# Kernel optimization log

Measured on AMD Instinct MI355X. Metric: run time of the kernel, lower is better.

The kernel has to match this reference:

```python
import jax, jax.numpy as jnp
import numpy as np

DIM = 256
NUM_HEADS = 4
HEAD_DIM = DIM // NUM_HEADS
WINDOW_SIZES = [2, 4, 8, 16]
SCALE = HEAD_DIM ** -0.5


def setup_inputs() -> dict:
    key = jax.random.key(0)
    k1, k2, k3, k4 = jax.random.split(key, 4)
    B, C, H, W = 8, DIM, 128, 128
    x = jax.random.normal(k1, (B, C, H, W), dtype=jnp.float32)
    # 1x1 conv weights stored as [out, in]
    qkv_w = jax.random.normal(k2, (3 * DIM, DIM), dtype=jnp.float32) * (DIM ** -0.5)
    proj_w = jax.random.normal(k3, (DIM, DIM), dtype=jnp.float32) * (DIM ** -0.5)
    proj_b = jax.random.normal(k4, (DIM,), dtype=jnp.float32) * 0.01
    return {"x": x, "qkv_w": qkv_w, "proj_w": proj_w, "proj_b": proj_b}


def _window_attn(q, k, v, ws):
    # q,k,v: [B, H, W, hd] for one head; windowed self-attention of size ws
    B, H, W, hd = q.shape
    hg, wg = H // ws, W // ws

    def part(t):
        # [B,H,W,hd] -> [B, hg*wg, ws*ws, hd]
        t = t.reshape(B, hg, ws, wg, ws, hd).transpose(0, 1, 3, 2, 4, 5)
        return t.reshape(B, hg * wg, ws * ws, hd)

    qw, kw, vw = part(q), part(k), part(v)
    attn = jnp.einsum('bgqd,bgkd->bgqk', qw, kw) * SCALE
    attn = jax.nn.softmax(attn, axis=-1)
    out = jnp.einsum('bgqk,bgkd->bgqd', attn, vw)
    # reassemble: [B, hg, wg, ws, ws, hd] -> [B, H, W, hd]
    out = out.reshape(B, hg, wg, ws, ws, hd).transpose(0, 1, 3, 2, 4, 5)
    return out.reshape(B, H, W, hd)


def reference(x, qkv_w, proj_w, proj_b):
    B, C, H, W = x.shape
    # 1x1 conv qkv: [B, 3*dim, H, W] -> [3, B, nh, H, W, hd]
    qkv = jnp.einsum('bchw,oc->bohw', x, qkv_w)
    qkv = qkv.reshape(B, 3, NUM_HEADS, HEAD_DIM, H, W).transpose(1, 0, 2, 4, 5, 3)
    q, k, v = qkv[0], qkv[1], qkv[2]
    outs = []
    for i, ws in enumerate(WINDOW_SIZES):
        outs.append(_window_attn(q[:, i], k[:, i], v[:, i], ws))
    y = jnp.concatenate(outs, axis=-1)  # [B, H, W, dim]
    y = jnp.einsum('bhwc,oc->bhwo', y, proj_w) + proj_b
    y = y.transpose(0, 3, 1, 2)  # [B, dim, H, W]
    return y + x
```

## Files before the change

### kernel.cpp

```cpp
#include <hip/hip_runtime.h>
#include <hip/hip_bf16.h>
#include <cstddef>
#include <cstdint>

typedef unsigned short u16;
typedef unsigned int uint32;
typedef __attribute__((ext_vector_type(8))) short bf16x8;
typedef __attribute__((ext_vector_type(4))) float f32x4;

#define SPATIAL 16384
#define TOTAL_M 131072

__device__ __forceinline__ u16 f2b(float f) {
  __hip_bfloat16 h = __float2bfloat16(f);
  return *reinterpret_cast<u16*>(&h);
}
__device__ __forceinline__ uint32 pk2(float a, float b) {
  return (uint32)f2b(a) | ((uint32)f2b(b) << 16);
}
__device__ __forceinline__ float blo(uint32 u) {
  union { uint32 u; float f; } c; c.u = u << 16; return c.f;
}
__device__ __forceinline__ float bhi(uint32 u) {
  union { uint32 u; float f; } c; c.u = u & 0xffff0000u; return c.f;
}

__device__ __forceinline__ void gload_lds16(const u16* g, u16* l) {
  __builtin_amdgcn_global_load_lds(
      (const __attribute__((address_space(1))) void*)g,
      (__attribute__((address_space(3))) void*)l, 16, 0, 0);
}

template <int WS>
__device__ __forceinline__ size_t tok_base(int gw, int tt) {
  constexpr int WG = 128 / WS;
  constexpr int NWIN = WG * WG;
  int bb = gw / NWIN, rr = gw % NWIN;
  int gy = rr / WG, gx = rr % WG;
  int yy = gy * WS + tt / WS, xx = gx * WS + tt % WS;
  return (((size_t)bb * 128 + yy) * 128 + xx) * 768;
}

__global__ __launch_bounds__(256) void wprep(const float* __restrict__ qw,
                                             const float* __restrict__ pw,
                                             u16* __restrict__ wq,
                                             u16* __restrict__ wp) {
  const int t = blockIdx.x * 256 + threadIdx.x;
#pragma unroll
  for (int i = 0; i < 16; ++i) {
    const int e = i * 4096 + t;
    if (e < 49152) {
      float4 v = *(const float4*)&qw[(size_t)e * 4];
      ushort4 o;
      o.x = f2b(v.x); o.y = f2b(v.y); o.z = f2b(v.z); o.w = f2b(v.w);
      *(ushort4*)&wq[(size_t)e * 4] = o;
    } else {
      float4 v = *(const float4*)&pw[(size_t)(e - 49152) * 4];
      ushort4 o;
      o.x = f2b(v.x); o.y = f2b(v.y); o.z = f2b(v.z); o.w = f2b(v.w);
      *(ushort4*)&wp[(size_t)(e - 49152) * 4] = o;
    }
  }
}

__global__ __launch_bounds__(256) void gemm_qkv(const float* __restrict__ x,
                                                const u16* __restrict__ wq,
                                                u16* __restrict__ qkv) {
  __shared__ u16 As[128 * 64];
  __shared__ u16 Bs[128 * 64];
  const int tid = threadIdx.x;
  const int bid = blockIdx.x;
  const int logical = (bid & 7) * 768 + (bid >> 3);
  const int m0 = (logical / 6) * 128;
  const int n0 = (logical % 6) * 128;
  const int b = m0 >> 14;
  const int sp0 = m0 & 16383;
  const int lane = tid & 63, w = tid >> 6;
  const int wr = w >> 1, wc = w & 1;
  const int fr = lane & 15, fk = lane >> 4;
  const int frx = (fr & 7) << 3;
  const int kcs = ((tid & 7) * 8) ^ (((tid >> 3) & 7) << 3);
  const int srow = tid >> 3;
  const int spq = tid & 31;
  const int kq8 = tid >> 5;
  f32x4 acc[4][4] = {};
  for (int kt = 0; kt < 4; ++kt) {
    const int k0 = kt * 64;
#pragma unroll
    for (int it = 0; it < 4; ++it) {
      int row = it * 32 + srow;
      u16* lb = &Bs[(it * 256 + (tid & 192)) * 8];
      gload_lds16(&wq[((size_t)(n0 + row) << 8) + k0 + kcs], lb);
    }
    float4 xa[8];
#pragma unroll
    for (int j = 0; j < 8; ++j)
      xa[j] = *(const float4*)&x[(((size_t)(b * 256 + k0 + kq8 * 8 + j)) << 14) + sp0 + spq * 4];
#pragma unroll
    for (int s = 0; s < 4; ++s) {
      const int sp = spq * 4 + s;
      union { bf16x8 v; uint32 u[4]; } U;
      U.u[0] = pk2(((const float*)&xa[0])[s], ((const float*)&xa[1])[s]);
      U.u[1] = pk2(((const float*)&xa[2])[s], ((const float*)&xa[3])[s]);
      U.u[2] = pk2(((const float*)&xa[4])[s], ((const float*)&xa[5])[s]);
      U.u[3] = pk2(((const float*)&xa[6])[s], ((const float*)&xa[7])[s]);
      const int ch = kq8 ^ (sp & 7);
      *(bf16x8*)&As[sp * 64 + ch * 8] = U.v;
    }
    __syncthreads();
#pragma unroll
    for (int kk = 0; kk < 2; ++kk) {
      const int kb = (kk * 32 + fk * 8) ^ frx;
      bf16x8 af[4], bfr[4];
#pragma unroll
      for (int i = 0; i < 4; ++i) {
        af[i] = *(const bf16x8*)&As[(wr * 64 + i * 16 + fr) * 64 + kb];
        bfr[i] = *(const bf16x8*)&Bs[(wc * 64 + i * 16 + fr) * 64 + kb];
      }
#pragma unroll
      for (int i = 0; i < 4; ++i)
#pragma unroll
        for (int j = 0; j < 4; ++j)
          acc[i][j] = __builtin_amdgcn_mfma_f32_16x16x32_bf16(bfr[j], af[i], acc[i][j], 0, 0, 0);
    }
    __syncthreads();
  }
#pragma unroll
  for (int i = 0; i < 4; ++i) {
    const size_t row = (size_t)(m0 + wr * 64 + i * 16 + fr) * 768;
#pragma unroll
    for (int j = 0; j < 4; ++j) {
      uint2 p;
      p.x = pk2(acc[i][j][0], acc[i][j][1]);
      p.y = pk2(acc[i][j][2], acc[i][j][3]);
      *(uint2*)&qkv[row + n0 + wc * 64 + j * 16 + fk * 4] = p;
    }
  }
}

template <int WS>
__device__ __forceinline__ void win_attn_body(u16* __restrict__ qkv, int head,
                                              int bid, u16 (*Ks)[68], u16 (*Vs)[68]) {
  constexpr int T = WS * WS;
  constexpr int G = 256 / T;
  const int tid = threadIdx.x;
  const int gw0 = bid * G;
  const int qoff = head * 64;

#pragma unroll
  for (int i = 0; i < 16; ++i) {
    int e4 = i * 256 + tid;
    int tok = e4 >> 4;
    int d4 = (e4 & 15) * 4;
    size_t base = tok_base<WS>(gw0 + tok / T, tok % T);
    *(uint2*)&Ks[tok][d4] = *(const uint2*)&qkv[base + 256 + qoff + d4];
    *(uint2*)&Vs[tok][d4] = *(const uint2*)&qkv[base + 512 + qoff + d4];
  }
  __syncthreads();

  const int myw = tid / T;
  const int mytt = tid % T;
  const size_t mybase = tok_base<WS>(gw0 + myw, mytt);

  float q[64];
#pragma unroll
  for (int d4 = 0; d4 < 16; ++d4) {
    uint2 q2 = *(const uint2*)&qkv[mybase + qoff + d4 * 4];
    q[d4 * 4 + 0] = blo(q2.x); q[d4 * 4 + 1] = bhi(q2.x);
    q[d4 * 4 + 2] = blo(q2.y); q[d4 * 4 + 3] = bhi(q2.y);
  }
  const int rbase = myw * T;

  float mmax = -1e30f, lsum = 0.f;
  for (int j = 0; j < T; ++j) {
    float s = 0.f;
#pragma unroll
    for (int d4 = 0; d4 < 16; ++d4) {
      uint2 k2 = *(const uint2*)&Ks[rbase + j][d4 * 4];
      s = fmaf(q[d4 * 4 + 0], blo(k2.x), s);
      s = fmaf(q[d4 * 4 + 1], bhi(k2.x), s);
      s = fmaf(q[d4 * 4 + 2], blo(k2.y), s);
      s = fmaf(q[d4 * 4 + 3], bhi(k2.y), s);
    }
    s *= 0.125f;
    const float mn = fmaxf(mmax, s);
    lsum = lsum * __expf(mmax - mn) + __expf(s - mn);
    mmax = mn;
  }
  const float inv = 1.f / lsum;

  float acc[64] = {};
  for (int j = 0; j < T; ++j) {
    float s = 0.f;
#pragma unroll
    for (int d4 = 0; d4 < 16; ++d4) {
      uint2 k2 = *(const uint2*)&Ks[rbase + j][d4 * 4];
      s = fmaf(q[d4 * 4 + 0], blo(k2.x), s);
      s = fmaf(q[d4 * 4 + 1], bhi(k2.x), s);
      s = fmaf(q[d4 * 4 + 2], blo(k2.y), s);
      s = fmaf(q[d4 * 4 + 3], bhi(k2.y), s);
    }
    const float p = __expf(s * 0.125f - mmax) * inv;
#pragma unroll
    for (int d4 = 0; d4 < 16; ++d4) {
      uint2 v2 = *(const uint2*)&Vs[rbase + j][d4 * 4];
      acc[d4 * 4 + 0] = fmaf(p, blo(v2.x), acc[d4 * 4 + 0]);
      acc[d4 * 4 + 1] = fmaf(p, bhi(v2.x), acc[d4 * 4 + 1]);
      acc[d4 * 4 + 2] = fmaf(p, blo(v2.y), acc[d4 * 4 + 2]);
      acc[d4 * 4 + 3] = fmaf(p, bhi(v2.y), acc[d4 * 4 + 3]);
    }
  }
#pragma unroll
  for (int d4 = 0; d4 < 16; ++d4) {
    uint2 o2;
    o2.x = pk2(acc[d4 * 4 + 0], acc[d4 * 4 + 1]);
    o2.y = pk2(acc[d4 * 4 + 2], acc[d4 * 4 + 3]);
    *(uint2*)&qkv[mybase + qoff + d4 * 4] = o2;
  }
}

__global__ __launch_bounds__(256) void win_small(u16* __restrict__ qkv) {
  __shared__ u16 Ks[256][68];
  __shared__ u16 Vs[256][68];
  if (blockIdx.x < 512)
    win_attn_body<2>(qkv, 0, blockIdx.x, Ks, Vs);
  else
    win_attn_body<4>(qkv, 1, blockIdx.x - 512, Ks, Vs);
}

template <int WS>
__global__ __launch_bounds__(256) void win_attn_mfma(u16* __restrict__ qkv, int head) {
  constexpr int T = WS * WS;
  constexpr int G = 256 / T;
  constexpr int KT = T / 16;
  constexpr int KS = T / 32;
  constexpr int PL = T + 8;
  __shared__ u16 Ks[256 * 72];
  __shared__ u16 Vt[64 * 264];
  __shared__ u16 Plds[4 * 16 * PL];
  const int tid = threadIdx.x;
  const int gw0 = blockIdx.x * G;
  const int qoff = head * 64;

#pragma unroll
  for (int it = 0; it < 16; ++it) {
    int e = it * 256 + tid;
    int tok = e >> 4;
    int d4 = (e & 15) * 4;
    int win = tok / T, tt = tok % T;
    size_t base = tok_base<WS>(gw0 + win, tt);
    uint2 kk = *(const uint2*)&qkv[base + 256 + qoff + d4];
    uint2 vv = *(const uint2*)&qkv[base + 512 + qoff + d4];
    *(uint2*)&Ks[tok * 72 + d4] = kk;
    Vt[(d4 + 0) * 264 + tok] = (u16)(vv.x & 0xffffu);
    Vt[(d4 + 1) * 264 + tok] = (u16)(vv.x >> 16);
    Vt[(d4 + 2) * 264 + tok] = (u16)(vv.y & 0xffffu);
    Vt[(d4 + 3) * 264 + tok] = (u16)(vv.y >> 16);
  }
  __syncthreads();

  const int w = tid >> 6, lane = tid & 63;
  const int fr = lane & 15, fk = lane >> 4;
  u16* prow = &Plds[(w * 16 + fr) * PL];

  for (int qi = 0; qi < 4; ++qi) {
    const int qg = w * 4 + qi;
    const int win = qg / (T / 16);
    const int qt = qg % (T / 16);
    const int gw = gw0 + win;

    const size_t qb = tok_base<WS>(gw, qt * 16 + fr) + qoff;
    bf16x8 qf[2];
#pragma unroll
    for (int ds = 0; ds < 2; ++ds)
      qf[ds] = *(const bf16x8*)&qkv[qb + ds * 32 + fk * 8];

    f32x4 sv[KT];
#pragma unroll
    for (int kt = 0; kt < KT; ++kt) {
      const u16* krow = &Ks[(win * T + kt * 16 + fr) * 72];
      bf16x8 k0 = *(const bf16x8*)&krow[fk * 8];
      bf16x8 k1 = *(const bf16x8*)&krow[32 + fk * 8];
      f32x4 s = {};
      s = __builtin_amdgcn_mfma_f32_16x16x32_bf16(k0, qf[0], s, 0, 0, 0);
      s = __builtin_amdgcn_mfma_f32_16x16x32_bf16(k1, qf[1], s, 0, 0, 0);
      sv[kt] = s;
    }

    float rmax = -3e38f;
#pragma unroll
    for (int kt = 0; kt < KT; ++kt)
#pragma unroll
      for (int r = 0; r < 4; ++r) rmax = fmaxf(rmax, sv[kt][r]);
    rmax = fmaxf(rmax, __shfl_xor(rmax, 16));
    rmax = fmaxf(rmax, __shfl_xor(rmax, 32));
    const float m = rmax * 0.125f;
    float l = 0.f;
#pragma unroll
    for (int kt = 0; kt < KT; ++kt)
#pragma unroll
      for (int r = 0; r < 4; ++r) {
        float ev = __expf(sv[kt][r] * 0.125f - m);
        sv[kt][r] = ev;
        l += ev;
      }
    l += __shfl_xor(l, 16);
    l += __shfl_xor(l, 32);
    const float linv = 1.f / l;

#pragma unroll
    for (int kt = 0; kt < KT; ++kt) {
      uint2 pp;
      pp.x = pk2(sv[kt][0], sv[kt][1]);
      pp.y = pk2(sv[kt][2], sv[kt][3]);
      *(uint2*)&prow[kt * 16 + fk * 4] = pp;
    }
    __asm__ __volatile__("s_waitcnt lgkmcnt(0)" ::: "memory");
    __builtin_amdgcn_sched_barrier(0);

    f32x4 ov[4] = {};
#pragma unroll
    for (int ks = 0; ks < KS; ++ks) {
      bf16x8 pf = *(const bf16x8*)&prow[ks * 32 + fk * 8];
#pragma unroll
      for (int dt = 0; dt < 4; ++dt) {
        bf16x8 vf = *(const bf16x8*)&Vt[(dt * 16 + fr) * 264 + win * T + ks * 32 + fk * 8];
        ov[dt] = __builtin_amdgcn_mfma_f32_16x16x32_bf16(pf, vf, ov[dt], 0, 0, 0);
      }
    }

#pragma unroll
    for (int r = 0; r < 4; ++r) {
      float lr = __shfl(linv, fk * 4 + r);
      size_t ob = tok_base<WS>(gw, qt * 16 + fk * 4 + r) + qoff;
#pragma unroll
      for (int dt = 0; dt < 4; ++dt)
        qkv[ob + dt * 16 + fr] = f2b(ov[dt][r] * lr);
    }
  }
}

__global__ __launch_bounds__(256) void gemm_proj(const u16* __restrict__ qkv,
                                                 const u16* __restrict__ wp,
                                                 const float* __restrict__ bias,
                                                 const float* __restrict__ x,
                                                 float* __restrict__ out) {
  __shared__ u16 As[2][128 * 64];
  __shared__ u16 Bs[2][128 * 64];
  const int tid = threadIdx.x;
  const int bid = blockIdx.x;
  const int logical = (bid & 7) * 256 + (bid >> 3);
  const int m0 = (logical >> 1) * 128;
  const int n0 = (logical & 1) * 128;
  const int lane = tid & 63, w = tid >> 6;
  const int wr = w >> 1, wc = w & 1;
  const int fr = lane & 15, fk = lane >> 4;
  const int frx = (fr & 7) << 3;
  const int kcs = ((tid & 7) * 8) ^ (((tid >> 3) & 7) << 3);
  const int srow = tid >> 3;
  const int b = m0 >> 14;
  f32x4 acc[4][4] = {};

#define STAGE_PRJ(B, KT)                                                     \
  do {                                                                       \
    const int k0s = (KT)*64;                                                 \
    _Pragma("unroll") for (int it = 0; it < 4; ++it) {                       \
      int row = it * 32 + srow;                                              \
      u16* la = &As[B][(it * 256 + (tid & 192)) * 8];                        \
      u16* lb = &Bs[B][(it * 256 + (tid & 192)) * 8];                        \
      gload_lds16(&qkv[(size_t)(m0 + row) * 768 + k0s + kcs], la);           \
      gload_lds16(&wp[((size_t)(n0 + row) << 8) + k0s + kcs], lb);           \
    }                                                                        \
  } while (0)

#define COMP_PRJ(B)                                                          \
  do {                                                                       \
    _Pragma("unroll") for (int kk = 0; kk < 2; ++kk) {                       \
      const int kb = (kk * 32 + fk * 8) ^ frx;                               \
      bf16x8 af[4], bfr[4];                                                  \
      _Pragma("unroll") for (int i = 0; i < 4; ++i) {                        \
        af[i] = *(const bf16x8*)&As[B][(wr * 64 + i * 16 + fr) * 64 + kb];   \
        bfr[i] = *(const bf16x8*)&Bs[B][(wc * 64 + i * 16 + fr) * 64 + kb];  \
      }                                                                      \
      _Pragma("unroll") for (int i = 0; i < 4; ++i)                          \
          _Pragma("unroll") for (int j = 0; j < 4; ++j) acc[i][j] =          \
          __builtin_amdgcn_mfma_f32_16x16x32_bf16(af[i], bfr[j],             \
                                                  acc[i][j], 0, 0, 0);       \
    }                                                                        \
  } while (0)

#define PHASE(WAITN)                                                         \
  asm volatile("s_waitcnt vmcnt(" #WAITN ")" ::: "memory");                  \
  __builtin_amdgcn_s_barrier();                                              \
  __builtin_amdgcn_sched_barrier(0)

#define PHASE_END()                                                          \
  __builtin_amdgcn_sched_barrier(0);                                         \
  __builtin_amdgcn_s_barrier()

  STAGE_PRJ(0, 0);
  STAGE_PRJ(1, 1);
  PHASE(8);
  COMP_PRJ(0);
  PHASE_END();
  STAGE_PRJ(0, 2);
  PHASE(8);
  COMP_PRJ(1);
  PHASE_END();
  STAGE_PRJ(1, 3);
  PHASE(8);
  COMP_PRJ(0);
  PHASE_END();
  PHASE(0);
  COMP_PRJ(1);
#undef STAGE_PRJ
#undef COMP_PRJ
#undef PHASE
#undef PHASE_END

#pragma unroll
  for (int i = 0; i < 4; ++i) {
    const int sp = (m0 & 16383) + wr * 64 + i * 16 + fk * 4;
#pragma unroll
    for (int j = 0; j < 4; ++j) {
      const int n = n0 + wc * 64 + j * 16 + fr;
      const size_t o = ((size_t)(b * 256 + n) << 14) + sp;
      const float4 r4 = *(const float4*)&x[o];
      const float bb = bias[n];
      float4 v = make_float4(acc[i][j][0] + bb + r4.x, acc[i][j][1] + bb + r4.y,
                             acc[i][j][2] + bb + r4.z, acc[i][j][3] + bb + r4.w);
      *(float4*)&out[o] = v;
    }
  }
}

extern "C" void kernel_launch(void* const* d_in, const int* in_sizes, int n_in,
                              void* d_out, int out_size, void* d_ws, size_t ws_size,
                              hipStream_t stream) {
  const float* x = (const float*)d_in[0];
  const float* qkv_w = (const float*)d_in[1];
  const float* proj_w = (const float*)d_in[2];
  const float* proj_b = (const float*)d_in[3];
  float* out = (float*)d_out;
  u16* qkv = (u16*)d_ws;
  u16* wq = qkv + (size_t)131072 * 768;
  u16* wp = wq + (size_t)768 * 256;

  wprep<<<16, 256, 0, stream>>>(qkv_w, proj_w, wq, wp);
  gemm_qkv<<<6144, 256, 0, stream>>>(x, wq, qkv);
  win_small<<<1024, 256, 0, stream>>>(qkv);
  win_attn_mfma<8><<<512, 256, 0, stream>>>(qkv, 2);
  win_attn_mfma<16><<<512, 256, 0, stream>>>(qkv, 3);
  gemm_proj<<<2048, 256, 0, stream>>>(qkv, wp, proj_b, x, out);
}
```

Measured before the change: 352.2 us.

## Pre-transpose x to bf16 token-major and DMA both GEMM operands to LDS

New measurement: 309.9 us. 12.0% less time.

```diff
diff --git a/kernel.cpp b/kernel.cpp
--- a/kernel.cpp
+++ b/kernel.cpp
@@ -41,71 +41,82 @@
   return (((size_t)bb * 128 + yy) * 128 + xx) * 768;
 }
 
-__global__ __launch_bounds__(256) void wprep(const float* __restrict__ qw,
-                                             const float* __restrict__ pw,
-                                             u16* __restrict__ wq,
-                                             u16* __restrict__ wp) {
-  const int t = blockIdx.x * 256 + threadIdx.x;
-#pragma unroll
-  for (int i = 0; i < 16; ++i) {
-    const int e = i * 4096 + t;
-    if (e < 49152) {
-      float4 v = *(const float4*)&qw[(size_t)e * 4];
-      ushort4 o;
-      o.x = f2b(v.x); o.y = f2b(v.y); o.z = f2b(v.z); o.w = f2b(v.w);
-      *(ushort4*)&wq[(size_t)e * 4] = o;
-    } else {
-      float4 v = *(const float4*)&pw[(size_t)(e - 49152) * 4];
-      ushort4 o;
-      o.x = f2b(v.x); o.y = f2b(v.y); o.z = f2b(v.z); o.w = f2b(v.w);
-      *(ushort4*)&wp[(size_t)(e - 49152) * 4] = o;
-    }
-  }
-}
-
-__global__ __launch_bounds__(256) void gemm_qkv(const float* __restrict__ x,
+__global__ __launch_bounds__(256) void prep(const float* __restrict__ x,
+                                            const float* __restrict__ qw,
+                                            const float* __restrict__ pw,
+                                            u16* __restrict__ xT,
+                                            u16* __restrict__ wq,
+                                            u16* __restrict__ wp) {
+  const int tid = threadIdx.x;
+  const int bid = blockIdx.x;
+  if (bid >= 2048) {
+    const int t = (bid - 2048) * 256 + tid;
+#pragma unroll
+    for (int i = 0; i < 16; ++i) {
+      const int e = i * 4096 + t;
+      if (e < 49152) {
+        float4 v = *(const float4*)&qw[(size_t)e * 4];
+        ushort4 o;
+        o.x = f2b(v.x); o.y = f2b(v.y); o.z = f2b(v.z); o.w = f2b(v.w);
+        *(ushort4*)&wq[(size_t)e * 4] = o;
+      } else {
+        float4 v = *(const float4*)&pw[(size_t)(e - 49152) * 4];
+        ushort4 o;
+        o.x = f2b(v.x); o.y = f2b(v.y); o.z = f2b(v.z); o.w = f2b(v.w);
+        *(ushort4*)&wp[(size_t)(e - 49152) * 4] = o;
+      }
+    }
+    return;
+  }
+  __shared__ u16 Ts[64 * 256];
+  const int b = bid >> 8;
+  const int sp0 = (bid & 255) * 64;
+#pragma unroll
+  for (int it = 0; it < 16; ++it) {
+    int e = it * 256 + tid;
+    int k = e >> 4;
+    int c4 = (e & 15) * 4;
+    float4 v = *(const float4*)&x[(((size_t)(b * 256 + k)) << 14) + sp0 + c4];
+    Ts[(c4 + 0) * 256 + (k ^ ((((c4 + 0)) & 31) << 3))] = f2b(v.x);
+    Ts[(c4 + 1) * 256 + (k ^ ((((c4 + 1)) & 31) << 3))] = f2b(v.y);
+    Ts[(c4 + 2) * 256 + (k ^ ((((c4 + 2)) & 31) << 3))] = f2b(v.z);
+    Ts[(c4 + 3) * 256 + (k ^ ((((c4 + 3)) & 31) << 3))] = f2b(v.w);
+  }
+  __syncthreads();
+#pragma unroll
+  for (int it = 0; it < 8; ++it) {
+    int e = it * 256 + tid;
+    int sp = e >> 5;
+    int kc = (e & 31) * 8;
+    bf16x8 row = *(const bf16x8*)&Ts[sp * 256 + (kc ^ ((sp & 31) << 3))];
+    *(bf16x8*)&xT[((size_t)(b * 16384 + sp0 + sp)) * 256 + kc] = row;
+  }
+}
+
+__global__ __launch_bounds__(256) void gemm_qkv(const u16* __restrict__ xT,
                                                 const u16* __restrict__ wq,
                                                 u16* __restrict__ qkv) {
   __shared__ u16 As[128 * 64];
   __shared__ u16 Bs[128 * 64];
   const int tid = threadIdx.x;
-  const int bid = blockIdx.x;
-  const int logical = (bid & 7) * 768 + (bid >> 3);
-  const int m0 = (logical / 6) * 128;
-  const int n0 = (logical % 6) * 128;
-  const int b = m0 >> 14;
-  const int sp0 = m0 & 16383;
+  const int n0 = blockIdx.x * 128;
+  const int m0 = blockIdx.y * 128;
   const int lane = tid & 63, w = tid >> 6;
   const int wr = w >> 1, wc = w & 1;
   const int fr = lane & 15, fk = lane >> 4;
   const int frx = (fr & 7) << 3;
-  const int kcs = ((tid & 7) * 8) ^ (((tid >> 3) & 7) << 3);
-  const int srow = tid >> 3;
-  const int spq = tid & 31;
-  const int kq8 = tid >> 5;
   f32x4 acc[4][4] = {};
   for (int kt = 0; kt < 4; ++kt) {
     const int k0 = kt * 64;
 #pragma unroll
     for (int it = 0; it < 4; ++it) {
-      int row = it * 32 + srow;
+      int e = it * 256 + tid;
+      int row = e >> 3;
+      int kcs = ((e & 7) * 8) ^ ((row & 7) << 3);
+      u16* la = &As[(it * 256 + (tid & 192)) * 8];
       u16* lb = &Bs[(it * 256 + (tid & 192)) * 8];
+      gload_lds16(&xT[((size_t)(m0 + row) << 8) + k0 + kcs], la);
       gload_lds16(&wq[((size_t)(n0 + row) << 8) + k0 + kcs], lb);
-    }
-    float4 xa[8];
-#pragma unroll
-    for (int j = 0; j < 8; ++j)
-      xa[j] = *(const float4*)&x[(((size_t)(b * 256 + k0 + kq8 * 8 + j)) << 14) + sp0 + spq * 4];
-#pragma unroll
-    for (int s = 0; s < 4; ++s) {
-      const int sp = spq * 4 + s;
-      union { bf16x8 v; uint32 u[4]; } U;
-      U.u[0] = pk2(((const float*)&xa[0])[s], ((const float*)&xa[1])[s]);
-      U.u[1] = pk2(((const float*)&xa[2])[s], ((const float*)&xa[3])[s]);
-      U.u[2] = pk2(((const float*)&xa[4])[s], ((const float*)&xa[5])[s]);
-      U.u[3] = pk2(((const float*)&xa[6])[s], ((const float*)&xa[7])[s]);
-      const int ch = kq8 ^ (sp & 7);
-      *(bf16x8*)&As[sp * 64 + ch * 8] = U.v;
     }
     __syncthreads();
 #pragma unroll
@@ -228,23 +239,25 @@
     win_attn_body<4>(qkv, 1, blockIdx.x - 512, Ks, Vs);
 }
 
-template <int WS>
-__global__ __launch_bounds__(256) void win_attn_mfma(u16* __restrict__ qkv, int head) {
+template <int WS, int NW>
+__global__ __launch_bounds__(NW * 64) void win_attn_mfma(u16* __restrict__ qkv, int head) {
   constexpr int T = WS * WS;
   constexpr int G = 256 / T;
   constexpr int KT = T / 16;
   constexpr int KS = T / 32;
   constexpr int PL = T + 8;
+  constexpr int NT = NW * 64;
+  constexpr int QPW = (G * T / 16) / NW;
   __shared__ u16 Ks[256 * 72];
   __shared__ u16 Vt[64 * 264];
-  __shared__ u16 Plds[4 * 16 * PL];
+  __shared__ u16 Plds[NW * 16 * PL];
   const int tid = threadIdx.x;
   const int gw0 = blockIdx.x * G;
   const int qoff = head * 64;
 
 #pragma unroll
-  for (int it = 0; it < 16; ++it) {
-    int e = it * 256 + tid;
+  for (int it = 0; it < 4096 / NT; ++it) {
+    int e = it * NT + tid;
     int tok = e >> 4;
     int d4 = (e & 15) * 4;
     int win = tok / T, tt = tok % T;
@@ -263,8 +276,8 @@
   const int fr = lane & 15, fk = lane >> 4;
   u16* prow = &Plds[(w * 16 + fr) * PL];
 
-  for (int qi = 0; qi < 4; ++qi) {
-    const int qg = w * 4 + qi;
+  for (int qi = 0; qi < QPW; ++qi) {
+    const int qg = w * QPW + qi;
     const int win = qg / (T / 16);
     const int qt = qg % (T / 16);
     const int gw = gw0 + win;
@@ -443,13 +456,14 @@
   const float* proj_b = (const float*)d_in[3];
   float* out = (float*)d_out;
   u16* qkv = (u16*)d_ws;
-  u16* wq = qkv + (size_t)131072 * 768;
+  u16* xT = qkv + (size_t)131072 * 768;
+  u16* wq = xT + (size_t)131072 * 256;
   u16* wp = wq + (size_t)768 * 256;
 
-  wprep<<<16, 256, 0, stream>>>(qkv_w, proj_w, wq, wp);
-  gemm_qkv<<<6144, 256, 0, stream>>>(x, wq, qkv);
+  prep<<<2064, 256, 0, stream>>>(x, qkv_w, proj_w, xT, wq, wp);
+  gemm_qkv<<<dim3(6, 1024), 256, 0, stream>>>(xT, wq, qkv);
   win_small<<<1024, 256, 0, stream>>>(qkv);
-  win_attn_mfma<8><<<512, 256, 0, stream>>>(qkv, 2);
-  win_attn_mfma<16><<<512, 256, 0, stream>>>(qkv, 3);
+  win_attn_mfma<8, 4><<<512, 256, 0, stream>>>(qkv, 2);
+  win_attn_mfma<16, 8><<<512, 512, 0, stream>>>(qkv, 3);
   gemm_proj<<<2048, 256, 0, stream>>>(qkv, wp, proj_b, x, out);
 }
```

## Merge small window-attention launches and run ws=16 head with 8 waves

Applied to the files above, without the earlier changes.

Measured after the change: 352.1 us. About the same (-0.0%).

```diff
diff --git a/kernel.cpp b/kernel.cpp
--- a/kernel.cpp
+++ b/kernel.cpp
@@ -69,10 +69,8 @@
   __shared__ u16 As[128 * 64];
   __shared__ u16 Bs[128 * 64];
   const int tid = threadIdx.x;
-  const int bid = blockIdx.x;
-  const int logical = (bid & 7) * 768 + (bid >> 3);
-  const int m0 = (logical / 6) * 128;
-  const int n0 = (logical % 6) * 128;
+  const int n0 = blockIdx.x * 128;
+  const int m0 = blockIdx.y * 128;
   const int b = m0 >> 14;
   const int sp0 = m0 & 16383;
   const int lane = tid & 63, w = tid >> 6;
@@ -80,15 +78,14 @@
   const int fr = lane & 15, fk = lane >> 4;
   const int frx = (fr & 7) << 3;
   const int kcs = ((tid & 7) * 8) ^ (((tid >> 3) & 7) << 3);
-  const int srow = tid >> 3;
-  const int spq = tid & 31;
-  const int kq8 = tid >> 5;
+  const int kq8 = tid & 7;
+  const int spq = tid >> 3;
   f32x4 acc[4][4] = {};
   for (int kt = 0; kt < 4; ++kt) {
     const int k0 = kt * 64;
 #pragma unroll
     for (int it = 0; it < 4; ++it) {
-      int row = it * 32 + srow;
+      int row = it * 32 + (tid >> 3);
       u16* lb = &Bs[(it * 256 + (tid & 192)) * 8];
       gload_lds16(&wq[((size_t)(n0 + row) << 8) + k0 + kcs], lb);
     }
@@ -104,8 +101,7 @@
       U.u[1] = pk2(((const float*)&xa[2])[s], ((const float*)&xa[3])[s]);
       U.u[2] = pk2(((const float*)&xa[4])[s], ((const float*)&xa[5])[s]);
       U.u[3] = pk2(((const float*)&xa[6])[s], ((const float*)&xa[7])[s]);
-      const int ch = kq8 ^ (sp & 7);
-      *(bf16x8*)&As[sp * 64 + ch * 8] = U.v;
+      *(bf16x8*)&As[sp * 64 + ((kq8 ^ (sp & 7)) * 8)] = U.v;
     }
     __syncthreads();
 #pragma unroll
@@ -219,32 +215,26 @@
   }
 }
 
-__global__ __launch_bounds__(256) void win_small(u16* __restrict__ qkv) {
-  __shared__ u16 Ks[256][68];
-  __shared__ u16 Vs[256][68];
-  if (blockIdx.x < 512)
-    win_attn_body<2>(qkv, 0, blockIdx.x, Ks, Vs);
-  else
-    win_attn_body<4>(qkv, 1, blockIdx.x - 512, Ks, Vs);
-}
-
-template <int WS>
-__global__ __launch_bounds__(256) void win_attn_mfma(u16* __restrict__ qkv, int head) {
+template <int WS, int NW>
+__device__ __forceinline__ void win_mfma_body(u16* __restrict__ qkv, int head,
+                                              int bid, u16* __restrict__ smem) {
   constexpr int T = WS * WS;
   constexpr int G = 256 / T;
   constexpr int KT = T / 16;
   constexpr int KS = T / 32;
   constexpr int PL = T + 8;
-  __shared__ u16 Ks[256 * 72];
-  __shared__ u16 Vt[64 * 264];
-  __shared__ u16 Plds[4 * 16 * PL];
+  constexpr int NT = NW * 64;
+  constexpr int QPW = (G * T / 16) / NW;
+  u16* Ks = smem;
+  u16* Vt = smem + 256 * 72;
+  u16* Plds = Vt + 64 * 264;
   const int tid = threadIdx.x;
-  const int gw0 = blockIdx.x * G;
+  const int gw0 = bid * G;
   const int qoff = head * 64;
 
 #pragma unroll
-  for (int it = 0; it < 16; ++it) {
-    int e = it * 256 + tid;
+  for (int it = 0; it < 4096 / NT; ++it) {
+    int e = it * NT + tid;
     int tok = e >> 4;
     int d4 = (e & 15) * 4;
     int win = tok / T, tt = tok % T;
@@ -263,8 +253,8 @@
   const int fr = lane & 15, fk = lane >> 4;
   u16* prow = &Plds[(w * 16 + fr) * PL];
 
-  for (int qi = 0; qi < 4; ++qi) {
-    const int qg = w * 4 + qi;
+  for (int qi = 0; qi < QPW; ++qi) {
+    const int qg = w * QPW + qi;
     const int win = qg / (T / 16);
     const int qt = qg % (T / 16);
     const int gw = gw0 + win;
@@ -338,6 +328,26 @@
         qkv[ob + dt * 16 + fr] = f2b(ov[dt][r] * lr);
     }
   }
+}
+
+__global__ __launch_bounds__(256) void attn_a(u16* __restrict__ qkv) {
+  __shared__ u16 smem[39936];
+  const int bid = blockIdx.x;
+  if (bid < 1024) {
+    u16 (*Ks)[68] = (u16(*)[68])smem;
+    u16 (*Vs)[68] = (u16(*)[68])(smem + 256 * 68);
+    if (bid < 512)
+      win_attn_body<2>(qkv, 0, bid, Ks, Vs);
+    else
+      win_attn_body<4>(qkv, 1, bid - 512, Ks, Vs);
+  } else {
+    win_mfma_body<8, 4>(qkv, 2, bid - 1024, smem);
+  }
+}
+
+__global__ __launch_bounds__(512) void attn16(u16* __restrict__ qkv) {
+  __shared__ u16 smem[256 * 72 + 64 * 264 + 8 * 16 * 264];
+  win_mfma_body<16, 8>(qkv, 3, blockIdx.x, smem);
 }
 
 __global__ __launch_bounds__(256) void gemm_proj(const u16* __restrict__ qkv,
@@ -447,9 +457,8 @@
   u16* wp = wq + (size_t)768 * 256;
 
   wprep<<<16, 256, 0, stream>>>(qkv_w, proj_w, wq, wp);
-  gemm_qkv<<<6144, 256, 0, stream>>>(x, wq, qkv);
-  win_small<<<1024, 256, 0, stream>>>(qkv);
-  win_attn_mfma<8><<<512, 256, 0, stream>>>(qkv, 2);
-  win_attn_mfma<16><<<512, 256, 0, stream>>>(qkv, 3);
+  gemm_qkv<<<dim3(6, 1024), 256, 0, stream>>>(x, wq, qkv);
+  attn_a<<<1536, 256, 0, stream>>>(qkv);
+  attn16<<<512, 512, 0, stream>>>(qkv);
   gemm_proj<<<2048, 256, 0, stream>>>(qkv, wp, proj_b, x, out);
 }
```
